# Kernel tuning notes

Hardware: AMD Instinct MI355X
Metric: run time of the kernel (lower is better)

The kernel has to match this reference:

```python
import jax, jax.numpy as jnp
import numpy as np

N, K, D = 65536, 1024, 512
INIT_COUNT = 100


def setup_inputs() -> dict:
    key = jax.random.key(0)
    k1, k2 = jax.random.split(key)
    embedded = jax.random.normal(k1, (N, D), dtype=jnp.float32)
    centers = jax.random.normal(k2, (K, D), dtype=jnp.float32)
    count = jnp.full((K,), INIT_COUNT, dtype=jnp.int32)  # start_training: ones(K)*100
    return {"embedded": embedded, "centers": centers, "count": count}


def reference(embedded, centers, count):
    # --- squared_euclidean_distance(centers, embedded): dist[n,k] = ||e_n - c_k||^2 ---
    e2 = jnp.sum(embedded * embedded, axis=-1, keepdims=True)   # [N,1]
    c2 = jnp.sum(centers * centers, axis=-1)                    # [K]
    cross = embedded @ centers.T                                # [N,K] GEMM
    dist = e2 + c2[None, :] - 2.0 * cross                       # [N,K]

    # compression_loss: min over clusters, then mean
    loss = jnp.mean(jnp.min(dist, axis=1))

    # prediction_hard: hard assignments
    s = jnp.argmin(dist, axis=1)                                # [N] int

    # update_centroids: the per-sample EMA with eta = 1/count[c] is exactly an
    # incremental (running) mean seeded with `count` pseudo-counts, so the
    # sequential loop is mathematically equivalent to a vectorized segment mean:
    #   new_centers[c] = (count[c]*centers[c] + sum_{s_i=c} e_i) / (count[c] + n_c)
    added = jax.ops.segment_sum(embedded, s, num_segments=K)                       # [K,D]
    n_add = jax.ops.segment_sum(jnp.ones_like(s, dtype=jnp.int32), s, num_segments=K)  # [K]
    new_count = count + n_add
    cf = count.astype(centers.dtype)[:, None]
    new_centers = (cf * centers + added) / new_count.astype(centers.dtype)[:, None]

    return loss, s, new_centers, new_count
```

## Files before the change

### kernel.cpp

```cpp
#include <hip/hip_runtime.h>

#define N_SAMPLES 65536
#define K_CENT    1024
#define DIM       512
#define TAU 0.125f

typedef __attribute__((ext_vector_type(8))) short  short8;
typedef _Float16 half8 __attribute__((ext_vector_type(8)));
typedef __attribute__((ext_vector_type(4))) float  float4v;

__device__ inline unsigned short f2h_bits(float x) {
    _Float16 h = (_Float16)x;
    return __builtin_bit_cast(unsigned short, h);
}

__global__ __launch_bounds__(256) void pack_kernel(const float* __restrict__ cen,
                                                   unsigned short* __restrict__ Bp,
                                                   float* __restrict__ c2) {
    const int wv = threadIdx.x >> 6, lane = threadIdx.x & 63;
    const int k = blockIdx.x * 4 + wv;
    const int kk = lane >> 2, quad = lane & 3;
    const float* src = cen + (size_t)k * DIM + kk * 32 + quad * 8;
    float4 v0 = *(const float4*)src;
    float4 v1 = *(const float4*)(src + 4);
    float f[8] = {v0.x, v0.y, v0.z, v0.w, v1.x, v1.y, v1.z, v1.w};
    short8 h;
    float s = 0.f;
    #pragma unroll
    for (int e = 0; e < 8; ++e) { h[e] = (short)f2h_bits(f[e]); s += f[e] * f[e]; }
    const int ntG = k >> 7, j4 = (k >> 4) & 7, l15 = k & 15;
    size_t slot = (size_t)(ntG * 16 + kk) * 512 + j4 * 64 + quad * 16 + l15;
    *(short8*)(Bp + slot * 8) = h;
    for (int off = 32; off; off >>= 1) s += __shfl_down(s, off);
    if (lane == 0) c2[k] = s;
}

__device__ inline void loadA(const float* aBase, int kc, float4v av[2][2]) {
    #pragma unroll
    for (int i = 0; i < 2; ++i) {
        const float4v* ap = (const float4v*)(aBase + (size_t)i * 16 * DIM + kc);
        av[i][0] = __builtin_nontemporal_load(ap);
        av[i][1] = __builtin_nontemporal_load(ap + 1);
    }
}

__device__ inline void cvtA1(const float4v av[2][2], half8 ah[2]) {
    #pragma unroll
    for (int i = 0; i < 2; ++i) {
        #pragma unroll
        for (int e = 0; e < 8; ++e)
            ah[i][e] = (_Float16)av[i][e >> 2][e & 3];
    }
}

__global__ __launch_bounds__(256, 4) void assign_mfma(
    const float* __restrict__ A,
    const unsigned short* __restrict__ Bp,
    const float* __restrict__ c2,
    float* __restrict__ pbest,
    float* __restrict__ psec,
    int* __restrict__ pidx)
{
    __shared__ float st_best[128];
    __shared__ float st_sec[128];
    __shared__ int   st_idx[128];

    const int tid  = threadIdx.x;
    const int w    = tid >> 6;
    const int lane = tid & 63;
    const int quad = lane >> 4;
    const int l15  = lane & 15;
    const int mblk  = blockIdx.x & 511;
    const int chunk = blockIdx.x >> 9;
    const int m0   = mblk * 128;

    if (tid < 128) { st_best[tid] = 3.4e38f; st_sec[tid] = 3.4e38f; st_idx[tid] = 0; }
    __syncthreads();

    const float* aBase = A + (size_t)(m0 + w * 32 + l15) * DIM + quad * 8;

    for (int nt = 0; nt < 4; ++nt) {
        const int ntG = chunk * 4 + nt;
        const int n0  = ntG * 128;
        const unsigned short* bBase = Bp + (size_t)ntG * 16 * 4096;

        float4v acc[16];
        #pragma unroll
        for (int z = 0; z < 16; ++z) acc[z] = (float4v){0.f, 0.f, 0.f, 0.f};

        float4v avN[2][2];
        half8 ah[2];
        loadA(aBase, 0, avN);
        cvtA1(avN, ah);

        for (int ks = 0; ks < 16; ++ks) {
            const unsigned short* bk = bBase + (size_t)ks * 4096;

            short8 br0 = *(const short8*)(bk + 0 * 512 + lane * 8);
            short8 br1 = *(const short8*)(bk + 1 * 512 + lane * 8);
            short8 br2 = *(const short8*)(bk + 2 * 512 + lane * 8);
            short8 br3 = *(const short8*)(bk + 3 * 512 + lane * 8);

            if (ks < 15) loadA(aBase, (ks + 1) * 32, avN);

            #pragma unroll
            for (int j4 = 0; j4 < 4; ++j4) {
                short8 braw = (j4 == 0) ? br0 : (j4 == 1) ? br1 : (j4 == 2) ? br2 : br3;
                half8 bh = __builtin_bit_cast(half8, braw);
                #pragma unroll
                for (int i = 0; i < 2; ++i)
                    acc[i * 8 + j4] = __builtin_amdgcn_mfma_f32_16x16x32_f16(
                        ah[i], bh, acc[i * 8 + j4], 0, 0, 0);
            }

            short8 br4 = *(const short8*)(bk + 4 * 512 + lane * 8);
            short8 br5 = *(const short8*)(bk + 5 * 512 + lane * 8);
            short8 br6 = *(const short8*)(bk + 6 * 512 + lane * 8);
            short8 br7 = *(const short8*)(bk + 7 * 512 + lane * 8);
            #pragma unroll
            for (int j4 = 4; j4 < 8; ++j4) {
                short8 braw = (j4 == 4) ? br4 : (j4 == 5) ? br5 : (j4 == 6) ? br6 : br7;
                half8 bh = __builtin_bit_cast(half8, braw);
                #pragma unroll
                for (int i = 0; i < 2; ++i)
                    acc[i * 8 + j4] = __builtin_amdgcn_mfma_f32_16x16x32_f16(
                        ah[i], bh, acc[i * 8 + j4], 0, 0, 0);
            }

            if (ks < 15) cvtA1(avN, ah);
        }

        float c2v[8];
        #pragma unroll
        for (int j = 0; j < 8; ++j) c2v[j] = c2[n0 + j * 16 + l15];
        #pragma unroll
        for (int i = 0; i < 2; ++i)
            #pragma unroll
            for (int reg = 0; reg < 4; ++reg) {
                float bv = 3.4e38f, sv = 3.4e38f; int bi = 0;
                #pragma unroll
                for (int j = 0; j < 8; ++j) {
                    float v = c2v[j] - 2.0f * acc[i * 8 + j][reg];
                    int n = n0 + j * 16 + l15;
                    if (v < bv) { sv = bv; bv = v; bi = n; }
                    else if (v < sv) sv = v;
                }
                #pragma unroll
                for (int mask = 1; mask < 16; mask <<= 1) {
                    float ob = __shfl_xor(bv, mask);
                    float os = __shfl_xor(sv, mask);
                    int   oi = __shfl_xor(bi, mask);
                    float ns = fminf(fminf(sv, os), fmaxf(bv, ob));
                    if (ob < bv || (ob == bv && oi < bi)) { bv = ob; bi = oi; }
                    sv = ns;
                }
                if (l15 == 0) {
                    int ml = w * 32 + i * 16 + quad * 4 + reg;
                    float sb = st_best[ml], ss = st_sec[ml]; int si = st_idx[ml];
                    float ns = fminf(fminf(ss, sv), fmaxf(sb, bv));
                    if (bv < sb || (bv == sb && bi < si)) { st_best[ml] = bv; st_idx[ml] = bi; }
                    st_sec[ml] = ns;
                }
            }
    }

    __syncthreads();
    if (tid < 128) {
        int m = m0 + tid;
        __builtin_nontemporal_store(st_best[tid], &pbest[chunk * N_SAMPLES + m]);
        __builtin_nontemporal_store(st_sec[tid],  &psec [chunk * N_SAMPLES + m]);
        __builtin_nontemporal_store(st_idx[tid],  &pidx [chunk * N_SAMPLES + m]);
    }
}

__global__ __launch_bounds__(256) void merge_kernel(
    const float* __restrict__ pbest,
    const float* __restrict__ psec,
    const int* __restrict__ pidx,
    int* __restrict__ s_idx,
    float* __restrict__ out_s,
    int* __restrict__ hist,
    int* __restrict__ flag_cnt,
    int* __restrict__ flagged,
    double* __restrict__ loss_d)
{
    int m = blockIdx.x * 256 + threadIdx.x;
    float b0 = pbest[m], b1 = pbest[N_SAMPLES + m];
    float s0 = psec[m],  s1 = psec[N_SAMPLES + m];
    int   i0 = pidx[m],  i1 = pidx[N_SAMPLES + m];
    float bv, sv; int bi;
    if (b1 < b0) { bv = b1; bi = i1; sv = fminf(b0, s1); }
    else         { bv = b0; bi = i0; sv = fminf(s0, b1); }
    s_idx[m] = bi;
    out_s[m] = (float)bi;
    atomicAdd(&hist[bi], 1);
    if (sv - bv < TAU) { int p = atomicAdd(flag_cnt, 1); flagged[p] = m; }

    float ls = bv;
    for (int off = 32; off; off >>= 1) ls += __shfl_down(ls, off);
    __shared__ float ws4[4];
    int lane = threadIdx.x & 63, wv = threadIdx.x >> 6;
    if (lane == 0) ws4[wv] = ls;
    __syncthreads();
    if (threadIdx.x == 0)
        atomicAdd(loss_d, (double)(ws4[0] + ws4[1] + ws4[2] + ws4[3]));
}

__global__ __launch_bounds__(256) void refine_kernel(
    const float* __restrict__ emb,
    const float* __restrict__ cen,
    const int* __restrict__ flag_cnt,
    const int* __restrict__ flagged,
    int* __restrict__ s_idx,
    float* __restrict__ out_s,
    int* __restrict__ hist)
{
    __shared__ float e_sh[DIM];
    __shared__ double rvd[256];
    __shared__ int rid[256];
    const int t = threadIdx.x;
    const int cnt = *flag_cnt;
    for (int idx = blockIdx.x; idx < cnt; idx += gridDim.x) {
        int n = flagged[idx];
        __syncthreads();
        ((float2*)e_sh)[t] = ((const float2*)(emb + (size_t)n * DIM))[t];
        __syncthreads();
        double bestd = 1e300;
        int bestk = 0;
        #pragma unroll
        for (int j = 0; j < 4; ++j) {
            int k = t * 4 + j;
            const float* crow = cen + (size_t)k * DIM;
            double acc = 0.0;
            for (int d = 0; d < DIM; d += 4) {
                float4 cv = *(const float4*)(crow + d);
                double d0 = (double)e_sh[d + 0] - (double)cv.x;
                double d1 = (double)e_sh[d + 1] - (double)cv.y;
                double d2 = (double)e_sh[d + 2] - (double)cv.z;
                double d3 = (double)e_sh[d + 3] - (double)cv.w;
                acc += d0 * d0 + d1 * d1 + d2 * d2 + d3 * d3;
            }
            if (acc < bestd) { bestd = acc; bestk = k; }
        }
        rvd[t] = bestd; rid[t] = bestk;
        __syncthreads();
        for (int off = 128; off; off >>= 1) {
            if (t < off) {
                double v = rvd[t + off]; int ii = rid[t + off];
                if (v < rvd[t] || (v == rvd[t] && ii < rid[t])) { rvd[t] = v; rid[t] = ii; }
            }
            __syncthreads();
        }
        if (t == 0) {
            int old = s_idx[n], nw = rid[0];
            if (nw != old) {
                atomicSub(&hist[old], 1);
                atomicAdd(&hist[nw], 1);
                s_idx[n] = nw;
                out_s[n] = (float)nw;
            }
        }
    }
}

__global__ void scan_kernel(const int* __restrict__ hist,
                            int* __restrict__ offsets,
                            int* __restrict__ cursor,
                            const int* __restrict__ count_in,
                            float* __restrict__ out_count) {
    __shared__ int sbuf[K_CENT];
    int t = threadIdx.x;
    int v = hist[t];
    sbuf[t] = v;
    __syncthreads();
    for (int off = 1; off < K_CENT; off <<= 1) {
        int x = (t >= off) ? sbuf[t - off] : 0;
        __syncthreads();
        sbuf[t] += x;
        __syncthreads();
    }
    int incl = sbuf[t];
    offsets[t] = incl - v;
    cursor[t]  = incl - v;
    out_count[t] = (float)(count_in[t] + v);
    if (t == K_CENT - 1) offsets[K_CENT] = incl;
}

__global__ void scatter_kernel(const int* __restrict__ s_idx,
                               int* __restrict__ cursor,
                               int* __restrict__ order) {
    int n = blockIdx.x * blockDim.x + threadIdx.x;
    if (n < N_SAMPLES) {
        int pos = atomicAdd(&cursor[s_idx[n]], 1);
        order[pos] = n;
    }
}

__global__ __launch_bounds__(256) void gp_kernel(
    const float* __restrict__ emb,
    const int* __restrict__ s_idx,
    const int* __restrict__ order,
    float* __restrict__ accum,
    double* __restrict__ loss_d)
{
    __shared__ int s_n[64], s_c[64];
    const int t = threadIdx.x;
    const int base = blockIdx.x * 64;
    if (t < 64) { int n = order[base + t]; s_n[t] = n; s_c[t] = s_idx[n]; }
    __syncthreads();
    float ax = 0.f, ay = 0.f, ssq = 0.f;
    int cur = s_c[0];
    for (int r = 0; r < 64; ++r) {
        int n = s_n[r], c = s_c[r];
        if (c != cur) {
            atomicAdd(&accum[(size_t)cur * DIM + t * 2], ax);
            atomicAdd(&accum[(size_t)cur * DIM + t * 2 + 1], ay);
            ax = ay = 0.f; cur = c;
        }
        float2 e = *(const float2*)(emb + (size_t)n * DIM + t * 2);
        ax += e.x; ay += e.y;
        ssq += e.x * e.x + e.y * e.y;
    }
    atomicAdd(&accum[(size_t)cur * DIM + t * 2], ax);
    atomicAdd(&accum[(size_t)cur * DIM + t * 2 + 1], ay);

    for (int off = 32; off; off >>= 1) ssq += __shfl_down(ssq, off);
    __shared__ float wsum[4];
    if ((t & 63) == 0) wsum[t >> 6] = ssq;
    __syncthreads();
    if (t == 0)
        atomicAdd(loss_d, (double)(wsum[0] + wsum[1] + wsum[2] + wsum[3]));
}

__global__ __launch_bounds__(256) void combine_kernel(
    const float* __restrict__ centers,
    const int* __restrict__ count_in,
    const int* __restrict__ hist,
    const float* __restrict__ accum,
    const double* __restrict__ loss_d,
    float* __restrict__ out_centers,
    float* __restrict__ out_loss)
{
    int k = blockIdx.x, t = threadIdx.x;
    if (k == 0 && t == 0) *out_loss = (float)(*loss_d * (1.0 / N_SAMPLES));
    float cn = (float)count_in[k];
    float tot = cn + (float)hist[k];
    float2 c = *(const float2*)(centers + (size_t)k * DIM + t * 2);
    float2 a = *(const float2*)(accum   + (size_t)k * DIM + t * 2);
    float2 o;
    o.x = (cn * c.x + a.x) / tot;
    o.y = (cn * c.y + a.y) / tot;
    *(float2*)(out_centers + (size_t)k * DIM + t * 2) = o;
}

extern "C" void kernel_launch(void* const* d_in, const int* in_sizes, int n_in,
                              void* d_out, int out_size, void* d_ws, size_t ws_size,
                              hipStream_t stream) {
    const float* emb = (const float*)d_in[0];
    const float* cen = (const float*)d_in[1];
    const int*   cnt = (const int*)d_in[2];

    float* out = (float*)d_out;
    float* out_loss    = out;
    float* out_s       = out + 1;
    float* out_centers = out + 1 + N_SAMPLES;
    float* out_count   = out + 1 + N_SAMPLES + (size_t)K_CENT * DIM;

    int* wsi = (int*)d_ws;
    int*   hist     = wsi;
    int*   offsets  = wsi + 1024;
    int*   cursor   = wsi + 2064;
    int*   s_idx    = wsi + 4096;
    float* c2       = (float*)(wsi + 69632);
    int*   flag_cnt = wsi + 70656;
    double* loss_d  = (double*)(wsi + 70712);
    int*   flagged  = wsi + 70720;
    float* pbest    = (float*)(wsi + 136256);
    float* psec     = (float*)(wsi + 267328);
    int*   pidx     = wsi + 398400;
    unsigned short* Bp = (unsigned short*)(wsi + 529472);
    int*   order    = wsi + 136256;
    float* accum    = (float*)(wsi + 529472);

    hipMemsetAsync(hist, 0, K_CENT * sizeof(int), stream);
    hipMemsetAsync(loss_d, 0, sizeof(double), stream);
    hipMemsetAsync(flag_cnt, 0, sizeof(int), stream);

    pack_kernel<<<256, 256, 0, stream>>>(cen, Bp, c2);
    assign_mfma<<<1024, 256, 0, stream>>>(emb, Bp, c2, pbest, psec, pidx);
    merge_kernel<<<N_SAMPLES / 256, 256, 0, stream>>>(pbest, psec, pidx, s_idx, out_s,
                                                      hist, flag_cnt, flagged, loss_d);
    hipMemsetAsync(accum, 0, (size_t)K_CENT * DIM * sizeof(float), stream);
    refine_kernel<<<256, 256, 0, stream>>>(emb, cen, flag_cnt, flagged, s_idx, out_s, hist);
    scan_kernel<<<1, K_CENT, 0, stream>>>(hist, offsets, cursor, cnt, out_count);
    scatter_kernel<<<N_SAMPLES / 256, 256, 0, stream>>>(s_idx, cursor, order);
    gp_kernel<<<N_SAMPLES / 64, 256, 0, stream>>>(emb, s_idx, order, accum, loss_d);
    combine_kernel<<<K_CENT, 256, 0, stream>>>(cen, cnt, hist, accum, loss_d,
                                               out_centers, out_loss);
}
```

Before: 727.7 us.

## Drop centroid-chunk split in assign kernel and double-buffer B fragment loads

The assign kernel now has each block cover all 1024 centroids instead of splitting them across two chunks. This halves the grid to 512 blocks and removes the two-way partial merge in merge_kernel. The B-fragment loads are double-buffered in registers across k-steps, and the next A slice is prefetched continuously across centroid tiles. The inner loop is fully unrolled, occupancy hints drop from 4 to 2 blocks per CU, and nontemporal loads and stores become normal accesses. The cost is higher register pressure and only 512 blocks, which may not fill the 256 CUs well.

```diff
diff --git a/kernel.cpp b/kernel.cpp
--- a/kernel.cpp
+++ b/kernel.cpp
@@ -39,8 +39,8 @@
     #pragma unroll
     for (int i = 0; i < 2; ++i) {
         const float4v* ap = (const float4v*)(aBase + (size_t)i * 16 * DIM + kc);
-        av[i][0] = __builtin_nontemporal_load(ap);
-        av[i][1] = __builtin_nontemporal_load(ap + 1);
+        av[i][0] = ap[0];
+        av[i][1] = ap[1];
     }
 }
 
@@ -53,7 +53,7 @@
     }
 }
 
-__global__ __launch_bounds__(256, 4) void assign_mfma(
+__global__ __launch_bounds__(256, 2) void assign_mfma(
     const float* __restrict__ A,
     const unsigned short* __restrict__ Bp,
     const float* __restrict__ c2,
@@ -70,64 +70,55 @@
     const int lane = tid & 63;
     const int quad = lane >> 4;
     const int l15  = lane & 15;
-    const int mblk  = blockIdx.x & 511;
-    const int chunk = blockIdx.x >> 9;
-    const int m0   = mblk * 128;
+    const int m0   = blockIdx.x * 128;
 
     if (tid < 128) { st_best[tid] = 3.4e38f; st_sec[tid] = 3.4e38f; st_idx[tid] = 0; }
     __syncthreads();
 
     const float* aBase = A + (size_t)(m0 + w * 32 + l15) * DIM + quad * 8;
 
-    for (int nt = 0; nt < 4; ++nt) {
-        const int ntG = chunk * 4 + nt;
-        const int n0  = ntG * 128;
-        const unsigned short* bBase = Bp + (size_t)ntG * 16 * 4096;
+    short8 br[2][8];
+    float4v avN[2][2];
+    half8 ah[2];
+
+    #pragma unroll
+    for (int j = 0; j < 8; ++j)
+        br[0][j] = *(const short8*)(Bp + j * 512 + lane * 8);
+    loadA(aBase, 0, avN);
+    cvtA1(avN, ah);
+
+    for (int nt = 0; nt < 8; ++nt) {
+        const int n0 = nt * 128;
 
         float4v acc[16];
         #pragma unroll
         for (int z = 0; z < 16; ++z) acc[z] = (float4v){0.f, 0.f, 0.f, 0.f};
 
-        float4v avN[2][2];
-        half8 ah[2];
-        loadA(aBase, 0, avN);
-        cvtA1(avN, ah);
-
+        #pragma unroll
         for (int ks = 0; ks < 16; ++ks) {
-            const unsigned short* bk = bBase + (size_t)ks * 4096;
-
-            short8 br0 = *(const short8*)(bk + 0 * 512 + lane * 8);
-            short8 br1 = *(const short8*)(bk + 1 * 512 + lane * 8);
-            short8 br2 = *(const short8*)(bk + 2 * 512 + lane * 8);
-            short8 br3 = *(const short8*)(bk + 3 * 512 + lane * 8);
-
-            if (ks < 15) loadA(aBase, (ks + 1) * 32, avN);
+            const int s   = nt * 16 + ks;
+            const int cur = ks & 1;
+            const int nxt = cur ^ 1;
+
+            {
+                const int sN = (s < 127) ? s + 1 : 127;
+                const unsigned short* bkN = Bp + (size_t)sN * 4096;
+                #pragma unroll
+                for (int j = 0; j < 8; ++j)
+                    br[nxt][j] = *(const short8*)(bkN + j * 512 + lane * 8);
+                loadA(aBase, ((ks + 1) & 15) * 32, avN);
+            }
 
             #pragma unroll
-            for (int j4 = 0; j4 < 4; ++j4) {
-                short8 braw = (j4 == 0) ? br0 : (j4 == 1) ? br1 : (j4 == 2) ? br2 : br3;
-                half8 bh = __builtin_bit_cast(half8, braw);
-                #pragma unroll
-                for (int i = 0; i < 2; ++i)
-                    acc[i * 8 + j4] = __builtin_amdgcn_mfma_f32_16x16x32_f16(
-                        ah[i], bh, acc[i * 8 + j4], 0, 0, 0);
-            }
-
-            short8 br4 = *(const short8*)(bk + 4 * 512 + lane * 8);
-            short8 br5 = *(const short8*)(bk + 5 * 512 + lane * 8);
-            short8 br6 = *(const short8*)(bk + 6 * 512 + lane * 8);
-            short8 br7 = *(const short8*)(bk + 7 * 512 + lane * 8);
-            #pragma unroll
-            for (int j4 = 4; j4 < 8; ++j4) {
-                short8 braw = (j4 == 4) ? br4 : (j4 == 5) ? br5 : (j4 == 6) ? br6 : br7;
-                half8 bh = __builtin_bit_cast(half8, braw);
-                #pragma unroll
-                for (int i = 0; i < 2; ++i)
-                    acc[i * 8 + j4] = __builtin_amdgcn_mfma_f32_16x16x32_f16(
-                        ah[i], bh, acc[i * 8 + j4], 0, 0, 0);
-            }
-
-            if (ks < 15) cvtA1(avN, ah);
+            for (int j4 = 0; j4 < 8; ++j4) {
+                half8 bh = __builtin_bit_cast(half8, br[cur][j4]);
+                acc[0 * 8 + j4] = __builtin_amdgcn_mfma_f32_16x16x32_f16(
+                    ah[0], bh, acc[0 * 8 + j4], 0, 0, 0);
+                acc[1 * 8 + j4] = __builtin_amdgcn_mfma_f32_16x16x32_f16(
+                    ah[1], bh, acc[1 * 8 + j4], 0, 0, 0);
+            }
+
+            cvtA1(avN, ah);
         }
 
         float c2v[8];
@@ -167,9 +158,9 @@
     __syncthreads();
     if (tid < 128) {
         int m = m0 + tid;
-        __builtin_nontemporal_store(st_best[tid], &pbest[chunk * N_SAMPLES + m]);
-        __builtin_nontemporal_store(st_sec[tid],  &psec [chunk * N_SAMPLES + m]);
-        __builtin_nontemporal_store(st_idx[tid],  &pidx [chunk * N_SAMPLES + m]);
+        pbest[m] = st_best[tid];
+        psec [m] = st_sec[tid];
+        pidx [m] = st_idx[tid];
     }
 }
 
@@ -185,12 +176,9 @@
     double* __restrict__ loss_d)
 {
     int m = blockIdx.x * 256 + threadIdx.x;
-    float b0 = pbest[m], b1 = pbest[N_SAMPLES + m];
-    float s0 = psec[m],  s1 = psec[N_SAMPLES + m];
-    int   i0 = pidx[m],  i1 = pidx[N_SAMPLES + m];
-    float bv, sv; int bi;
-    if (b1 < b0) { bv = b1; bi = i1; sv = fminf(b0, s1); }
-    else         { bv = b0; bi = i0; sv = fminf(s0, b1); }
+    float bv = pbest[m];
+    float sv = psec[m];
+    int   bi = pidx[m];
     s_idx[m] = bi;
     out_s[m] = (float)bi;
     atomicAdd(&hist[bi], 1);
@@ -387,7 +375,7 @@
     hipMemsetAsync(flag_cnt, 0, sizeof(int), stream);
 
     pack_kernel<<<256, 256, 0, stream>>>(cen, Bp, c2);
-    assign_mfma<<<1024, 256, 0, stream>>>(emb, Bp, c2, pbest, psec, pidx);
+    assign_mfma<<<512, 256, 0, stream>>>(emb, Bp, c2, pbest, psec, pidx);
     merge_kernel<<<N_SAMPLES / 256, 256, 0, stream>>>(pbest, psec, pidx, s_idx, out_s,
                                                       hist, flag_cnt, flagged, loss_d);
     hipMemsetAsync(accum, 0, (size_t)K_CENT * DIM * sizeof(float), stream);
```

After: 684.8 us. 5.9% less time.
